# Performance work log

Measured on AMD Instinct MI355X. Metric: run time of the kernel, lower is better.

Reference implementation:

```python
import jax, jax.numpy as jnp
import numpy as np

LATENT, TARGET, EMB_SCALE = 2048, 64, 0.1
STEPS_IGNORE, STEPS_PREDICT = 2, 3


def conv(x, w, b, stride=(1, 1), padding=((0, 0), (0, 0))):
    y = jax.lax.conv_general_dilated(x, w, stride, padding,
                                     dimension_numbers=('NCHW', 'OIHW', 'NCHW'))
    return y + b[None, :, None, None]


def setup_inputs() -> dict:
    key = jax.random.key(0)
    ks = jax.random.split(key, 24)
    B = 64
    inp = {}
    inp['images'] = jax.random.normal(ks[0], (B, 3, 256, 256), jnp.float32)
    inp['rnd'] = jax.random.randint(ks[1], (B * 49,), 0, 16, jnp.int32)
    s = lambda *sh: 1.0 / np.sqrt(np.prod(sh[1:]))
    # stand-in encoder: conv3->256 k8 s8, relu, conv256->2048 1x1, relu, global mean pool
    inp['enc_w1'] = jax.random.normal(ks[2], (256, 3, 8, 8), jnp.float32) * s(256, 3, 8, 8)
    inp['enc_b1'] = jnp.zeros((256,), jnp.float32)
    inp['enc_w2'] = jax.random.normal(ks[3], (LATENT, 256, 1, 1), jnp.float32) * s(LATENT, 256)
    inp['enc_b2'] = jnp.zeros((LATENT,), jnp.float32)
    # PixelCNN: 5 residual blocks, each 4 convs
    inp['pc_w1'] = jax.random.normal(ks[4], (5, 256, LATENT, 1, 1), jnp.float32) * s(0, LATENT)
    inp['pc_b1'] = jnp.zeros((5, 256), jnp.float32)
    inp['pc_w2'] = jax.random.normal(ks[5], (5, 256, 256, 1, 3), jnp.float32) * s(0, 256 * 3)
    inp['pc_b2'] = jnp.zeros((5, 256), jnp.float32)
    inp['pc_w3'] = jax.random.normal(ks[6], (5, 256, 256, 2, 1), jnp.float32) * s(0, 256 * 2)
    inp['pc_b3'] = jnp.zeros((5, 256), jnp.float32)
    inp['pc_w4'] = jax.random.normal(ks[7], (5, LATENT, 256, 1, 1), jnp.float32) * s(0, 256)
    inp['pc_b4'] = jnp.zeros((5, LATENT), jnp.float32)
    inp['z2t_w'] = jax.random.normal(ks[8], (TARGET, LATENT, 1, 1), jnp.float32) * s(0, LATENT)
    inp['z2t_b'] = jnp.zeros((TARGET,), jnp.float32)
    inp['c2p_w'] = jax.random.normal(ks[9], (STEPS_PREDICT, TARGET, LATENT, 1, 1), jnp.float32) * s(0, LATENT)
    inp['c2p_b'] = jnp.zeros((STEPS_PREDICT, TARGET), jnp.float32)
    return inp


def _forward(images, enc_w1, enc_b1, enc_w2, enc_b2,
             pc_w1, pc_b1, pc_w2, pc_b2, pc_w3, pc_b3, pc_w4, pc_b4,
             z2t_w, z2t_b, c2p_w, c2p_b, rnd):
    B = images.shape[0]
    # ---- patch extraction: (B,3,256,256) -> (B*49,3,64,64), r-major then c ----
    patches = jnp.stack([images[:, :, r * 32:r * 32 + 64, c * 32:c * 32 + 64]
                         for r in range(7) for c in range(7)], axis=1)
    patches = patches.reshape(-1, 3, 64, 64)
    N = patches.shape[0]
    # ---- vectorized random border masking (replaces per-patch python loop) ----
    r = (rnd // 4).astype(jnp.int32)           # (N,)
    c = (rnd % 4).astype(jnp.int32)
    idx = jnp.arange(64, dtype=jnp.int32)
    row_ok = (idx[None, :] >= r[:, None]) & (idx[None, :] < r[:, None] + 60)  # (N,64)
    col_ok = (idx[None, :] >= c[:, None]) & (idx[None, :] < c[:, None] + 60)
    mask = row_ok[:, None, :, None] & col_ok[:, None, None, :]                # (N,1,64,64)
    patches = jnp.where(mask, patches, jnp.float32(-1.0))
    # ---- stand-in encoder (resnet_v1 replaced by small conv stack) ----
    h = jax.nn.relu(conv(patches, enc_w1, enc_b1, stride=(8, 8)))  # (N,256,8,8)
    h = jax.nn.relu(conv(h, enc_w2, enc_b2))                        # (N,2048,8,8)
    latents = h.mean(axis=(2, 3))                                   # (N,2048)
    latents = latents.reshape(B, 7, 7, LATENT).transpose(0, 3, 1, 2)  # (B,2048,7,7)
    # ---- PixelCNN context ----
    x = latents
    for k in range(5):
        y = jax.nn.relu(conv(x, pc_w1[k], pc_b1[k]))
        y = jax.nn.relu(conv(y, pc_w2[k], pc_b2[k], padding=((0, 0), (1, 1))))
        y = jax.nn.relu(conv(y, pc_w3[k], pc_b3[k], padding=((1, 0), (0, 0))))
        y = conv(y, pc_w4[k], pc_b4[k])
        x = jax.nn.relu(y + x)
    context = x
    # ---- contrastive loss ----
    targets = conv(latents, z2t_w, z2t_b).transpose(0, 2, 3, 1).reshape(-1, TARGET)  # (B*49,64)
    col_dim, row_dim = 7, 7
    loss = jnp.float32(0.0)
    for i in range(STEPS_IGNORE, STEPS_IGNORE + STEPS_PREDICT):
        col_dim_i = col_dim - i - 1
        total = B * col_dim_i * row_dim
        preds = conv(context, c2p_w[i - STEPS_IGNORE], c2p_b[i - STEPS_IGNORE])
        preds = preds[:, :, :-(i + 1), :] * EMB_SCALE
        preds = preds.transpose(0, 2, 3, 1).reshape(-1, TARGET)  # (total,64)
        logits = preds @ targets.T                                # (total, B*49)
        ar = jnp.arange(total)
        b_idx = ar // (col_dim_i * row_dim)
        col = ar % (col_dim_i * row_dim)
        labels = b_idx * (col_dim * row_dim) + (i + 1) * row_dim + col
        lsm = jax.nn.log_softmax(logits, axis=-1)
        loss = loss + (-lsm[ar, labels]).mean()
    return loss, latents.mean(axis=(2, 3))


def reference(images, rnd, enc_w1, enc_b1, enc_w2, enc_b2,
              pc_w1, pc_b1, pc_w2, pc_b2, pc_w3, pc_b3, pc_w4, pc_b4,
              z2t_w, z2t_b, c2p_w, c2p_b):
    return _forward(images, enc_w1, enc_b1, enc_w2, enc_b2,
                    pc_w1, pc_b1, pc_w2, pc_b2, pc_w3, pc_b3, pc_w4, pc_b4,
                    z2t_w, z2t_b, c2p_w, c2p_b, rnd)
```

## Files before the change

### kernel.cpp

```cpp
#include <hip/hip_runtime.h>
#include <hip/hip_bf16.h>
#include <cstdint>
#include <cstddef>

typedef __attribute__((ext_vector_type(8))) short short8;
typedef __attribute__((ext_vector_type(4))) short short4v;
typedef __attribute__((ext_vector_type(4))) float f32x4;

__device__ __forceinline__ float bf2f(unsigned short u) {
  union { unsigned int i; float f; } v; v.i = ((unsigned int)u) << 16; return v.f;
}
__device__ __forceinline__ unsigned short f2bf(float f) {
  union { float f; unsigned int i; } v; v.f = f;
  unsigned int x = v.i;
  return (unsigned short)((x + 0x7fffu + ((x >> 16) & 1u)) >> 16);
}
__device__ __forceinline__ f32x4 mfma16(short8 a, short8 b, f32x4 c) {
  return __builtin_amdgcn_mfma_f32_16x16x32_bf16(a, b, c, 0, 0, 0);
}
__device__ __forceinline__ void gload16(const void* src, void* dst) {
  __builtin_amdgcn_global_load_lds(
      (const __attribute__((address_space(1))) unsigned int*)src,
      (__attribute__((address_space(3))) unsigned int*)dst, 16, 0, 0);
}

__device__ __forceinline__ void cvt4(const float* __restrict__ src,
                                     unsigned short* __restrict__ dst, int i) {
  float4 v = reinterpret_cast<const float4*>(src)[i];
  short4v o;
  o[0] = (short)f2bf(v.x); o[1] = (short)f2bf(v.y);
  o[2] = (short)f2bf(v.z); o[3] = (short)f2bf(v.w);
  reinterpret_cast<short4v*>(dst)[i] = o;
}

__global__ __launch_bounds__(256) void k_prep(
    const float* __restrict__ enc_w1, const float* __restrict__ enc_w2,
    const float* __restrict__ pc_w1, const float* __restrict__ pc_w4,
    const float* __restrict__ z2t_w, const float* __restrict__ c2p_w,
    const float* __restrict__ pc_w2, const float* __restrict__ pc_w3,
    unsigned short* __restrict__ w1b, unsigned short* __restrict__ w2b,
    unsigned short* __restrict__ pcw1b, unsigned short* __restrict__ pcw4b,
    unsigned short* __restrict__ z2tb, unsigned short* __restrict__ c2pb,
    unsigned short* __restrict__ w2t, unsigned short* __restrict__ w3t)
{
  const int b = blockIdx.x, tid = threadIdx.x;
  if (b < 48)        cvt4(enc_w1, w1b,   b * 256 + tid);
  else if (b < 560)  cvt4(enc_w2, w2b,   (b - 48) * 256 + tid);
  else if (b < 3120) cvt4(pc_w1,  pcw1b, (b - 560) * 256 + tid);
  else if (b < 5680) cvt4(pc_w4,  pcw4b, (b - 3120) * 256 + tid);
  else if (b < 5808) cvt4(z2t_w,  z2tb,  (b - 5680) * 256 + tid);
  else if (b < 6192) cvt4(c2p_w,  c2pb,  (b - 5808) * 256 + tid);
  else if (b < 10032) {
    const int e = (b - 6192) * 256 + tid;
    const int k5 = e / 196608, r = e % 196608;
    const int co = r / 768, kk = r % 768, d = kk >> 8, ci = kk & 255;
    w2t[e] = f2bf(pc_w2[((size_t)(k5 * 256 + co) * 256 + ci) * 3 + d]);
  } else {
    const int e = (b - 10032) * 256 + tid;
    const int k5 = e / 131072, r = e % 131072;
    const int co = r >> 9, kk = r & 511, s = kk >> 8, ci = kk & 255;
    w3t[e] = f2bf(pc_w3[((size_t)(k5 * 256 + co) * 256 + ci) * 2 + s]);
  }
}

__global__ __launch_bounds__(256) void k_enc2(
    const unsigned short* __restrict__ H1, const unsigned short* __restrict__ w2b,
    const float* __restrict__ b2, unsigned short* __restrict__ xout, int gbase)
{
  __shared__ char lds[32768];
  char* At = lds;
  char* Bt = lds + 16384;
  const int tid = threadIdx.x;
  const int nwg = gridDim.x;
  int bid = blockIdx.x;
  int l = bid;
  if ((nwg & 7) == 0) { const int cpx = nwg >> 3; l = (bid & 7) * cpx + (bid >> 3); }
  const int m0 = (l & 15) * 128;
  const int by = l >> 4;
  const int w = tid >> 6, lane = tid & 63, lr = lane & 15, lg = lane >> 4;
  const int wm = w & 1, wn = w >> 1;
  const int srow = lane >> 3, sslot = lane & 7;
  f32x4 acc[4][4];
  for (int i = 0; i < 4; i++) for (int j = 0; j < 4; j++) acc[i][j] = (f32x4)0.f;
  for (int kb = 0; kb < 4; kb++) {
    __syncthreads();
#pragma unroll
    for (int c = 0; c < 4; c++) {
      const int rbase = w * 32 + c * 8;
      const int row = rbase + srow;
      gload16(w2b + (size_t)(m0 + row) * 256 + kb * 64 + ((sslot ^ (row & 7)) * 8),
              At + rbase * 128);
    }
#pragma unroll
    for (int c = 0; c < 4; c++) {
      const int rbase = w * 32 + c * 8;
      const int row = rbase + srow;
      gload16(H1 + (size_t)(by * 128 + row) * 256 + kb * 64 + ((sslot ^ (row & 7)) * 8),
              Bt + rbase * 128);
    }
    __syncthreads();
#pragma unroll
    for (int kk = 0; kk < 2; kk++) {
      const int gg = kk * 4 + lg;
      short8 bb[4];
#pragma unroll
      for (int nt = 0; nt < 4; nt++) {
        const int row = wn * 64 + nt * 16 + lr;
        bb[nt] = *reinterpret_cast<const short8*>(Bt + row * 128 + ((gg ^ (row & 7)) * 16));
      }
#pragma unroll
      for (int cot = 0; cot < 4; cot++) {
        const int row = wm * 64 + cot * 16 + lr;
        const short8 a = *reinterpret_cast<const short8*>(At + row * 128 + ((gg ^ (row & 7)) * 16));
#pragma unroll
        for (int nt = 0; nt < 4; nt++)
          acc[cot][nt] = mfma16(a, bb[nt], acc[cot][nt]);
      }
    }
  }
  const int n = gbase + by * 2 + wn;
#pragma unroll
  for (int cot = 0; cot < 4; cot++) {
    const int cob = m0 + wm * 64 + cot * 16 + lg * 4;
    float4 bi = *reinterpret_cast<const float4*>(b2 + cob);
    const float bv[4] = { bi.x, bi.y, bi.z, bi.w };
    float s[4] = { 0.f, 0.f, 0.f, 0.f };
#pragma unroll
    for (int nt = 0; nt < 4; nt++)
#pragma unroll
      for (int r = 0; r < 4; r++)
        s[r] += fmaxf(acc[cot][nt][r] + bv[r], 0.f);
#pragma unroll
    for (int r = 0; r < 4; r++)
#pragma unroll
      for (int mk = 1; mk < 16; mk <<= 1)
        s[r] += __shfl_xor(s[r], mk, 64);
    if (lr == 0) {
      short4v o;
#pragma unroll
      for (int r = 0; r < 4; r++) o[r] = (short)f2bf(s[r] * (1.f / 64.f));
      *reinterpret_cast<short4v*>(xout + (size_t)n * 2048 + cob) = o;
    }
  }
}

__global__ __launch_bounds__(256) void k_out2(const unsigned short* __restrict__ x,
                                              float* __restrict__ out) {
  const int ch = blockIdx.x * 256 + threadIdx.x;
  const int b = blockIdx.y;
  float s = 0.f;
  for (int p = 0; p < 49; p++) s += bf2f(x[(size_t)(b * 49 + p) * 2048 + ch]);
  out[1 + b * 2048 + ch] = s * (1.f / 49.f);
}

template<int M_BLK, int BK, int MODE, bool BIAS, bool RELU, bool RESID, bool SCALE, bool OBF16>
__global__ __launch_bounds__(256) void k_gemm(
    const unsigned short* __restrict__ in, const unsigned short* __restrict__ W,
    const float* __restrict__ bias, float* __restrict__ outf,
    unsigned short* __restrict__ outb, const unsigned short* __restrict__ res,
    int M, int K, int bstride, int aux, float scale,
    int wzs, int bzs, int ozs,
    const float* __restrict__ img, const int* __restrict__ rndp)
{
  constexpr int MF = M_BLK / 64;
  constexpr int GPR = BK / 8;
  constexpr int ROWS = 64 / GPR;
  constexpr int RS = BK * 2;
  constexpr int CHA = (M_BLK / 4) / ROWS;
  constexpr int CHB = 16 / ROWS;
  constexpr int AG = M_BLK * 8;
  constexpr bool DBUF = (MODE == 0);
  constexpr int BUF = (M_BLK + 64) * RS;
  __shared__ char ldsb[(DBUF ? 2 : 1) * BUF];
  const int tid = threadIdx.x;
  const int z = blockIdx.z;
  W += (size_t)z * wzs;
  if (BIAS) bias += (size_t)z * bzs;
  const int m0 = blockIdx.x * M_BLK;
  const int n0 = blockIdx.y * 64;
  const int w = tid >> 6, lane = tid & 63, lr = lane & 15, lg = lane >> 4;
  const int srow = lane / GPR, sslot = lane % GPR;
  int pb = 0, pR = 0, pC = 0, roff = 0, coff = 0;
  if constexpr (MODE == 4) {
    const int pn = aux + blockIdx.y;
    pb = pn / 49; const int prc = pn % 49; pR = prc / 7; pC = prc % 7;
    const int rv = rndp[pn];
    roff = rv >> 2; coff = rv & 3;
  }
  f32x4 acc[MF][4];
  for (int mf = 0; mf < MF; mf++) for (int nt = 0; nt < 4; nt++) acc[mf][nt] = (f32x4)0.f;
  const int KB = K / BK;

  auto stageA = [&](char* At, int kb) {
#pragma unroll
    for (int c = 0; c < CHA; c++) {
      const int rbase = w * (M_BLK / 4) + c * ROWS;
      const int row = rbase + srow;
      gload16(W + (size_t)(m0 + row) * K + kb * BK + ((sslot ^ (row & 7)) * 8),
              At + rbase * RS);
    }
  };
  auto compute = [&](const char* At, const char* Bt) {
#pragma unroll
    for (int kk = 0; kk < BK / 32; kk++) {
      short8 a[MF], bb[4];
      const int gg = kk * 4 + lg;
#pragma unroll
      for (int mf = 0; mf < MF; mf++) {
        const int row = w * (M_BLK / 4) + mf * 16 + lr;
        a[mf] = *reinterpret_cast<const short8*>(At + row * RS + ((gg ^ (row & 7)) * 16));
      }
#pragma unroll
      for (int nt = 0; nt < 4; nt++) {
        const int row = nt * 16 + lr;
        bb[nt] = *reinterpret_cast<const short8*>(Bt + row * RS + ((gg ^ (row & 7)) * 16));
      }
#pragma unroll
      for (int mf = 0; mf < MF; mf++)
#pragma unroll
        for (int nt = 0; nt < 4; nt++)
          acc[mf][nt] = mfma16(a[mf], bb[nt], acc[mf][nt]);
    }
  };

  if constexpr (DBUF) {
    auto stageB = [&](char* Bt, int kb) {
#pragma unroll
      for (int c = 0; c < CHB; c++) {
        const int rbase = w * 16 + c * ROWS;
        const int row = rbase + srow;
        const int n = n0 + row;
        gload16(in + (size_t)n * bstride + kb * BK + ((sslot ^ (row & 7)) * 8),
                Bt + rbase * RS);
      }
    };
    stageA(ldsb, 0);
    stageB(ldsb + M_BLK * RS, 0);
    __syncthreads();
    int cur = 0;
    for (int kb = 0; kb < KB; kb++) {
      if (kb + 1 < KB) {
        char* nb = ldsb + (cur ^ 1) * BUF;
        stageA(nb, kb + 1);
        stageB(nb + M_BLK * RS, kb + 1);
      }
      char* cb = ldsb + cur * BUF;
      compute(cb, cb + M_BLK * RS);
      __syncthreads();
      cur ^= 1;
    }
  } else {
    for (int kb = 0; kb < KB; kb++) {
      __syncthreads();
      stageA(ldsb, kb);
      char* Bt = ldsb + M_BLK * RS;
      for (int g = AG + tid; g < AG + 512; g += 256) {
        const int h = g - AG, row = h >> 3, slot = h & 7;
        const int n = n0 + row;
        const int k = kb * 64 + slot * 8;
        short8 v = (short8)(short)0;
        if constexpr (MODE == 1) {
          const int d = k >> 8, ci = k & 255;
          const int wp = n % 7 + d - 1;
          if ((unsigned)wp <= 6u)
            v = *reinterpret_cast<const short8*>(in + (size_t)(n + d - 1) * 256 + ci);
        } else if constexpr (MODE == 2) {
          const int s2 = k >> 8, ci = k & 255;
          const int hh = (n % 49) / 7;
          if (hh + s2 >= 1)
            v = *reinterpret_cast<const short8*>(in + (size_t)(n + (s2 - 1) * 7) * 256 + ci);
        } else {
          const int p = row;
          const int gr = kb * 8 + slot;
          const int ci = gr >> 3, ky = gr & 7;
          const int oy = p >> 3, ox = p & 7;
          const int y = oy * 8 + ky;
          const float* src = img + (((size_t)(pb * 3 + ci) * 256 + (size_t)(pR * 32 + y)) * 256
                                    + pC * 32 + ox * 8);
          float4 v0 = *reinterpret_cast<const float4*>(src);
          float4 v1 = *reinterpret_cast<const float4*>(src + 4);
          const bool rok = (y >= roff) && (y < roff + 60);
          float vals[8] = { v0.x, v0.y, v0.z, v0.w, v1.x, v1.y, v1.z, v1.w };
          const int x0 = ox * 8;
#pragma unroll
          for (int q = 0; q < 8; q++) {
            const int xx = x0 + q;
            const bool ok = rok && (xx >= coff) && (xx < coff + 60);
            v[q] = (short)f2bf(ok ? vals[q] : -1.0f);
          }
        }
        *reinterpret_cast<short8*>(Bt + row * RS + ((slot ^ (row & 7)) * 16)) = v;
      }
      __syncthreads();
      compute(ldsb, ldsb + M_BLK * RS);
    }
  }

#pragma unroll
  for (int mf = 0; mf < MF; mf++) {
    const int mb = m0 + w * (M_BLK / 4) + mf * 16 + lg * 4;
    float bv[4] = {0.f, 0.f, 0.f, 0.f};
    if constexpr (BIAS) {
      float4 t4 = *reinterpret_cast<const float4*>(bias + mb);
      bv[0] = t4.x; bv[1] = t4.y; bv[2] = t4.z; bv[3] = t4.w;
    }
#pragma unroll
    for (int nt = 0; nt < 4; nt++) {
      const size_t nn = (size_t)(n0 + nt * 16 + lr);
      const size_t off = nn * (size_t)M + mb + (size_t)z * ozs;
      float v[4];
#pragma unroll
      for (int r = 0; r < 4; r++) {
        v[r] = acc[mf][nt][r] + bv[r];
        if (SCALE) v[r] *= scale;
      }
      if (RESID) {
        short4v rv = *reinterpret_cast<const short4v*>(res + off);
#pragma unroll
        for (int r = 0; r < 4; r++) v[r] += bf2f((unsigned short)rv[r]);
      }
#pragma unroll
      for (int r = 0; r < 4; r++) if (RELU) v[r] = fmaxf(v[r], 0.f);
      if (OBF16) {
        short4v o;
#pragma unroll
        for (int r = 0; r < 4; r++) o[r] = (short)f2bf(v[r]);
        *reinterpret_cast<short4v*>(outb + off) = o;
      } else {
        float4 o; o.x = v[0]; o.y = v[1]; o.z = v[2]; o.w = v[3];
        *reinterpret_cast<float4*>(outf + off) = o;
      }
    }
  }
}

__global__ __launch_bounds__(256) void k_lse2(
    const unsigned short* __restrict__ predsb, const unsigned short* __restrict__ targ,
    float* __restrict__ pm, float* __restrict__ ps, float* __restrict__ zlab)
{
  __shared__ char At[8192];
  __shared__ char Bt[8192];
  __shared__ float redM[4][64], redS[4][64];
  const int tid = threadIdx.x;
  const int R0 = blockIdx.x * 64;
  const int tz = blockIdx.y;
  const int t0 = tz * 13;
  const int t1 = (t0 + 13 < 49) ? (t0 + 13) : 49;
  int ip, base, cd7;
  if (R0 < 1792)      { ip = 0; base = 0;    cd7 = 28; }
  else if (R0 < 3136) { ip = 1; base = 1792; cd7 = 21; }
  else                { ip = 2; base = 3136; cd7 = 14; }
  const int lab7 = 7 * (ip + 3);
  const unsigned short* preds = predsb + (size_t)ip * 200704;
  const int w = tid >> 6, lane = tid & 63, lr = lane & 15, lg = lane >> 4;
  const int srow = lane >> 3, sslot = lane & 7;

#pragma unroll
  for (int c = 0; c < 2; c++) {
    const int rbase = w * 16 + c * 8;
    const int row = rbase + srow;
    const int rr = R0 - base + row;
    const int np = (rr / cd7) * 49 + (rr % cd7);
    gload16(preds + (size_t)np * 64 + ((sslot ^ (row & 7)) * 8), Bt + rbase * 128);
  }

  int labv[4];
#pragma unroll
  for (int nt = 0; nt < 4; nt++) {
    const int nc = R0 - base + nt * 16 + lr;
    labv[nt] = (nc / cd7) * 49 + (nc % cd7) + lab7;
  }
  float mrun[4] = {-1e30f, -1e30f, -1e30f, -1e30f};
  float srun[4] = {0.f, 0.f, 0.f, 0.f};

  for (int t = t0; t < t1; t++) {
#pragma unroll
    for (int c = 0; c < 2; c++) {
      const int rbase = w * 16 + c * 8;
      const int row = rbase + srow;
      gload16(targ + (size_t)(t * 64 + row) * 64 + ((sslot ^ (row & 7)) * 8),
              At + rbase * 128);
    }
    __syncthreads();
    f32x4 av[4];
#pragma unroll
    for (int nt = 0; nt < 4; nt++) av[nt] = (f32x4)0.f;
#pragma unroll
    for (int kk = 0; kk < 2; kk++) {
      const int gg = kk * 4 + lg;
      const int arow = w * 16 + lr;
      const short8 a = *reinterpret_cast<const short8*>(At + arow * 128 + ((gg ^ (arow & 7)) * 16));
#pragma unroll
      for (int nt = 0; nt < 4; nt++) {
        const int brow = nt * 16 + lr;
        const short8 b = *reinterpret_cast<const short8*>(Bt + brow * 128 + ((gg ^ (brow & 7)) * 16));
        av[nt] = mfma16(a, b, av[nt]);
      }
    }
    const int mg = t * 64 + w * 16 + lg * 4;
#pragma unroll
    for (int nt = 0; nt < 4; nt++) {
      float v0 = av[nt][0], v1 = av[nt][1], v2 = av[nt][2], v3 = av[nt][3];
      if (mg + 0 == labv[nt]) zlab[R0 + nt * 16 + lr] = v0;
      if (mg + 1 == labv[nt]) zlab[R0 + nt * 16 + lr] = v1;
      if (mg + 2 == labv[nt]) zlab[R0 + nt * 16 + lr] = v2;
      if (mg + 3 == labv[nt]) zlab[R0 + nt * 16 + lr] = v3;
      const float vm = fmaxf(fmaxf(v0, v1), fmaxf(v2, v3));
      const float nm = fmaxf(mrun[nt], vm);
      srun[nt] = srun[nt] * __expf(mrun[nt] - nm)
               + __expf(v0 - nm) + __expf(v1 - nm) + __expf(v2 - nm) + __expf(v3 - nm);
      mrun[nt] = nm;
    }
    __syncthreads();
  }
#pragma unroll
  for (int nt = 0; nt < 4; nt++) {
#pragma unroll
    for (int mk = 16; mk < 64; mk <<= 1) {
      const float om = __shfl_xor(mrun[nt], mk, 64);
      const float os = __shfl_xor(srun[nt], mk, 64);
      const float nm = fmaxf(mrun[nt], om);
      srun[nt] = srun[nt] * __expf(mrun[nt] - nm) + os * __expf(om - nm);
      mrun[nt] = nm;
    }
    if (lg == 0) { redM[w][nt * 16 + lr] = mrun[nt]; redS[w][nt * 16 + lr] = srun[nt]; }
  }
  __syncthreads();
  if (tid < 64) {
    float m = redM[0][tid], s = redS[0][tid];
#pragma unroll
    for (int wv = 1; wv < 4; wv++) {
      const float om = redM[wv][tid], os = redS[wv][tid];
      const float nm = fmaxf(m, om);
      s = s * __expf(m - nm) + os * __expf(om - nm);
      m = nm;
    }
    pm[(R0 + tid) * 4 + tz] = m;
    ps[(R0 + tid) * 4 + tz] = s;
  }
}

__global__ __launch_bounds__(256) void k_loss_final(
    const float* __restrict__ pm, const float* __restrict__ ps,
    const float* __restrict__ zlab, float* __restrict__ out)
{
  __shared__ float red[256];
  const int tid = threadIdx.x;
  float acc = 0.f;
  for (int i = tid; i < 4032; i += 256) {
    float m = pm[i * 4], s = ps[i * 4];
#pragma unroll
    for (int j = 1; j < 4; j++) {
      const float om = pm[i * 4 + j], os = ps[i * 4 + j];
      const float nm = fmaxf(m, om);
      s = s * __expf(m - nm) + os * __expf(om - nm);
      m = nm;
    }
    const float loss = (m + __logf(s)) - zlab[i];
    const float wgt = (i < 1792) ? (1.f / 1792.f) : ((i < 3136) ? (1.f / 1344.f) : (1.f / 896.f));
    acc += loss * wgt;
  }
  red[tid] = acc;
  for (int off = 128; off > 0; off >>= 1) {
    __syncthreads();
    if (tid < off) red[tid] += red[tid + off];
  }
  if (tid == 0) out[0] = red[0];
}

extern "C" void kernel_launch(void* const* d_in, const int* in_sizes, int n_in,
                              void* d_out, int out_size, void* d_ws, size_t ws_size,
                              hipStream_t stream)
{
  (void)in_sizes; (void)n_in; (void)out_size;
  const float* images = (const float*)d_in[0];
  const int*   rnd    = (const int*)d_in[1];
  const float* enc_w1 = (const float*)d_in[2];
  const float* enc_b1 = (const float*)d_in[3];
  const float* enc_w2 = (const float*)d_in[4];
  const float* enc_b2 = (const float*)d_in[5];
  const float* pc_w1  = (const float*)d_in[6];
  const float* pc_b1  = (const float*)d_in[7];
  const float* pc_w2  = (const float*)d_in[8];
  const float* pc_b2  = (const float*)d_in[9];
  const float* pc_w3  = (const float*)d_in[10];
  const float* pc_b3  = (const float*)d_in[11];
  const float* pc_w4  = (const float*)d_in[12];
  const float* pc_b4  = (const float*)d_in[13];
  const float* z2t_w  = (const float*)d_in[14];
  const float* z2t_b  = (const float*)d_in[15];
  const float* c2p_w  = (const float*)d_in[16];
  const float* c2p_b  = (const float*)d_in[17];
  float* out = (float*)d_out;
  char* ws = (char*)d_ws;

  unsigned short* w1b    = (unsigned short*)(ws + 0);
  unsigned short* w2b    = (unsigned short*)(ws + 98304);
  unsigned short* z2tb   = (unsigned short*)(ws + 1146880);
  unsigned short* c2pb   = (unsigned short*)(ws + 1409024);
  unsigned short* w2t    = (unsigned short*)(ws + 2195456);
  unsigned short* w3t    = (unsigned short*)(ws + 4161536);
  unsigned short* targ   = (unsigned short*)(ws + 5472256);
  unsigned short* predsb = (unsigned short*)(ws + 5873664);
  unsigned short* y1b    = (unsigned short*)(ws + 7094016);
  unsigned short* y2b    = (unsigned short*)(ws + 8699648);
  unsigned short* pcw1b  = (unsigned short*)(ws + 10305280);
  unsigned short* pcw4b  = (unsigned short*)(ws + 15548160);
  unsigned short* xbuf   = (unsigned short*)(ws + 20791040);
  float*          pm     = (float*)(ws + 7094016);
  float*          psum   = (float*)(ws + 7158528);
  float*          zlab   = (float*)(ws + 7223040);

  k_prep<<<12592, 256, 0, stream>>>(enc_w1, enc_w2, pc_w1, pc_w4, z2t_w, c2p_w,
                                    pc_w2, pc_w3,
                                    w1b, w2b, pcw1b, pcw4b, z2tb, c2pb, w2t, w3t);

  const size_t h1_off = 33636352;
  const size_t per_patch = 64 * 256 * 2;
  unsigned short* H1;
  int CH;
  if (ws_size > h1_off + 2 * per_patch) {
    size_t avail = (ws_size - h1_off) / per_patch;
    CH = (int)(avail > 3136 ? 3136 : avail) & ~1;
    H1 = (unsigned short*)(ws + h1_off);
  } else {
    H1 = y1b;
    CH = 98;
  }
  for (int base = 0; base < 3136; base += CH) {
    const int c = (3136 - base) < CH ? (3136 - base) : CH;
    k_gemm<256, 64, 4, true, true, false, false, true><<<dim3(1, c), 256, 0, stream>>>(
        nullptr, w1b, enc_b1, nullptr, H1, nullptr, 256, 192, 0, base, 1.f,
        0, 0, 0, images, rnd);
    k_enc2<<<16 * (c / 2), 256, 0, stream>>>(H1, w2b, enc_b2, xbuf, base);
  }

  k_out2<<<dim3(8, 64), 256, 0, stream>>>(xbuf, out);
  k_gemm<64, 128, 0, true, false, false, false, true><<<dim3(1, 49), 256, 0, stream>>>(
      xbuf, z2tb, z2t_b, nullptr, targ, nullptr, 64, 2048, 2048, 0, 1.f, 0, 0, 0,
      nullptr, nullptr);

  for (int k = 0; k < 5; k++) {
    k_gemm<64, 128, 0, true, true, false, false, true><<<dim3(4, 49), 256, 0, stream>>>(
        xbuf, pcw1b + (size_t)k * 524288, pc_b1 + k * 256, nullptr, y1b, nullptr,
        256, 2048, 2048, 0, 1.f, 0, 0, 0, nullptr, nullptr);
    k_gemm<64, 64, 1, true, true, false, false, true><<<dim3(4, 49), 256, 0, stream>>>(
        y1b, w2t + (size_t)k * 196608, pc_b2 + k * 256, nullptr, y2b, nullptr,
        256, 768, 256, 0, 1.f, 0, 0, 0, nullptr, nullptr);
    k_gemm<64, 64, 2, true, true, false, false, true><<<dim3(4, 49), 256, 0, stream>>>(
        y2b, w3t + (size_t)k * 131072, pc_b3 + k * 256, nullptr, y1b, nullptr,
        256, 512, 256, 0, 1.f, 0, 0, 0, nullptr, nullptr);
    k_gemm<128, 64, 0, true, true, true, false, true><<<dim3(16, 49), 256, 0, stream>>>(
        y1b, pcw4b + (size_t)k * 524288, pc_b4 + k * 2048, nullptr, xbuf, xbuf,
        2048, 256, 256, 0, 1.f, 0, 0, 0, nullptr, nullptr);
  }

  k_gemm<64, 128, 0, true, false, false, true, true><<<dim3(1, 49, 3), 256, 0, stream>>>(
      xbuf, c2pb, c2p_b, nullptr, predsb, nullptr, 64, 2048, 2048, 0, 0.1f,
      131072, 64, 200704, nullptr, nullptr);

  k_lse2<<<dim3(63, 4), 256, 0, stream>>>(predsb, targ, pm, psum, zlab);
  k_loss_final<<<1, 256, 0, stream>>>(pm, psum, zlab, out);
}
```

Baseline: 639.5 us.

## Fuse PixelCNN conv2/conv3 per image, stream enc2 weights from global, widen LSE split

Adds a k_conv23 kernel that computes the 1x3 and 2x1 convolutions for one image in a single block, keeping the intermediate activation in LDS so the y2 global round trip and one launch per residual block go away. In k_enc2 the weight tile is no longer staged through LDS; MFMA A operands are read directly from global memory, which halves LDS use. k_lse2 now splits the target dimension into 7 chunks instead of 4 for more parallelism, and the fallback chunk size for the encoder changes. The fused conv kernel runs only 64 blocks, which may underuse the GPU, and the direct global weight reads rely on cache hits.

Measured after the change: 893.1 us. 39.7% more time.

```diff
diff --git a/kernel.cpp b/kernel.cpp
--- a/kernel.cpp
+++ b/kernel.cpp
@@ -67,9 +67,7 @@
     const unsigned short* __restrict__ H1, const unsigned short* __restrict__ w2b,
     const float* __restrict__ b2, unsigned short* __restrict__ xout, int gbase)
 {
-  __shared__ char lds[32768];
-  char* At = lds;
-  char* Bt = lds + 16384;
+  __shared__ char Bt[16384];
   const int tid = threadIdx.x;
   const int nwg = gridDim.x;
   int bid = blockIdx.x;
@@ -88,13 +86,6 @@
     for (int c = 0; c < 4; c++) {
       const int rbase = w * 32 + c * 8;
       const int row = rbase + srow;
-      gload16(w2b + (size_t)(m0 + row) * 256 + kb * 64 + ((sslot ^ (row & 7)) * 8),
-              At + rbase * 128);
-    }
-#pragma unroll
-    for (int c = 0; c < 4; c++) {
-      const int rbase = w * 32 + c * 8;
-      const int row = rbase + srow;
       gload16(H1 + (size_t)(by * 128 + row) * 256 + kb * 64 + ((sslot ^ (row & 7)) * 8),
               Bt + rbase * 128);
     }
@@ -110,8 +101,9 @@
       }
 #pragma unroll
       for (int cot = 0; cot < 4; cot++) {
-        const int row = wm * 64 + cot * 16 + lr;
-        const short8 a = *reinterpret_cast<const short8*>(At + row * 128 + ((gg ^ (row & 7)) * 16));
+        const int co = m0 + wm * 64 + cot * 16 + lr;
+        const short8 a = *reinterpret_cast<const short8*>(
+            w2b + (size_t)co * 256 + kb * 64 + kk * 32 + lg * 8);
 #pragma unroll
         for (int nt = 0; nt < 4; nt++)
           acc[cot][nt] = mfma16(a, bb[nt], acc[cot][nt]);
@@ -151,6 +143,124 @@
   float s = 0.f;
   for (int p = 0; p < 49; p++) s += bf2f(x[(size_t)(b * 49 + p) * 2048 + ch]);
   out[1 + b * 2048 + ch] = s * (1.f / 49.f);
+}
+
+__global__ __launch_bounds__(256) void k_conv23(
+    const unsigned short* __restrict__ y1, const unsigned short* __restrict__ w2t,
+    const float* __restrict__ b2, const unsigned short* __restrict__ w3t,
+    const float* __restrict__ b3, unsigned short* __restrict__ y3)
+{
+  __shared__ char Bst[8192];
+  __shared__ char y2l[32768];
+  const int tid = threadIdx.x;
+  const int b = blockIdx.x;
+  const int nb = b * 49;
+  const int w = tid >> 6, lane = tid & 63, lr = lane & 15, lg = lane >> 4;
+  f32x4 acc[4][4];
+  for (int i = 0; i < 4; i++) for (int j = 0; j < 4; j++) acc[i][j] = (f32x4)0.f;
+
+  for (int kb = 0; kb < 12; kb++) {
+    __syncthreads();
+    for (int g = tid; g < 512; g += 256) {
+      const int row = g >> 3, slot = g & 7;
+      const int k = kb * 64 + slot * 8;
+      const int d = k >> 8, ci = k & 255;
+      short8 v = (short8)(short)0;
+      if (row < 49) {
+        const int wc = row % 7 + d - 1;
+        if ((unsigned)wc <= 6u)
+          v = *reinterpret_cast<const short8*>(y1 + (size_t)(nb + row + d - 1) * 256 + ci);
+      }
+      *reinterpret_cast<short8*>(Bst + row * 128 + ((slot ^ (row & 7)) * 16)) = v;
+    }
+    __syncthreads();
+#pragma unroll
+    for (int kk = 0; kk < 2; kk++) {
+      const int gg = kk * 4 + lg;
+      short8 bb[4];
+#pragma unroll
+      for (int nt = 0; nt < 4; nt++) {
+        const int row = nt * 16 + lr;
+        bb[nt] = *reinterpret_cast<const short8*>(Bst + row * 128 + ((gg ^ (row & 7)) * 16));
+      }
+#pragma unroll
+      for (int cot = 0; cot < 4; cot++) {
+        const int co = w * 64 + cot * 16 + lr;
+        const short8 a = *reinterpret_cast<const short8*>(
+            w2t + (size_t)co * 768 + kb * 64 + kk * 32 + lg * 8);
+#pragma unroll
+        for (int nt = 0; nt < 4; nt++)
+          acc[cot][nt] = mfma16(a, bb[nt], acc[cot][nt]);
+      }
+    }
+  }
+#pragma unroll
+  for (int cot = 0; cot < 4; cot++) {
+    const int cob = w * 64 + cot * 16 + lg * 4;
+    float4 bi = *reinterpret_cast<const float4*>(b2 + cob);
+    const float bv[4] = { bi.x, bi.y, bi.z, bi.w };
+    const int g2 = cob >> 3;
+#pragma unroll
+    for (int nt = 0; nt < 4; nt++) {
+      const int row = nt * 16 + lr;
+      short4v o;
+#pragma unroll
+      for (int r = 0; r < 4; r++)
+        o[r] = (short)f2bf(fmaxf(acc[cot][nt][r] + bv[r], 0.f));
+      const int sw = (g2 & ~7) | ((g2 & 7) ^ (row & 7));
+      *reinterpret_cast<short4v*>(y2l + row * 512 + sw * 16 + (cob & 7) * 2) = o;
+    }
+  }
+  __syncthreads();
+
+  f32x4 ac2[4][4];
+  for (int i = 0; i < 4; i++) for (int j = 0; j < 4; j++) ac2[i][j] = (f32x4)0.f;
+  for (int kb = 0; kb < 8; kb++) {
+    const int soff = (kb >= 4) ? 0 : -7;
+#pragma unroll
+    for (int kk = 0; kk < 2; kk++) {
+      const int gg = kk * 4 + lg;
+      const int gci = (kb * 8 + gg) & 31;
+      short8 bb[4];
+#pragma unroll
+      for (int nt = 0; nt < 4; nt++) {
+        const int nout = nt * 16 + lr;
+        const int ry = nout + soff;
+        short8 v = (short8)(short)0;
+        if (ry >= 0) {
+          const int sw = (gci & ~7) | ((gci & 7) ^ (ry & 7));
+          v = *reinterpret_cast<const short8*>(y2l + ry * 512 + sw * 16);
+        }
+        bb[nt] = v;
+      }
+#pragma unroll
+      for (int cot = 0; cot < 4; cot++) {
+        const int co = w * 64 + cot * 16 + lr;
+        const short8 a = *reinterpret_cast<const short8*>(
+            w3t + (size_t)co * 512 + kb * 64 + kk * 32 + lg * 8);
+#pragma unroll
+        for (int nt = 0; nt < 4; nt++)
+          ac2[cot][nt] = mfma16(a, bb[nt], ac2[cot][nt]);
+      }
+    }
+  }
+#pragma unroll
+  for (int cot = 0; cot < 4; cot++) {
+    const int cob = w * 64 + cot * 16 + lg * 4;
+    float4 bi = *reinterpret_cast<const float4*>(b3 + cob);
+    const float bv[4] = { bi.x, bi.y, bi.z, bi.w };
+#pragma unroll
+    for (int nt = 0; nt < 4; nt++) {
+      const int nout = nt * 16 + lr;
+      if (nout < 49) {
+        short4v o;
+#pragma unroll
+        for (int r = 0; r < 4; r++)
+          o[r] = (short)f2bf(fmaxf(ac2[cot][nt][r] + bv[r], 0.f));
+        *reinterpret_cast<short4v*>(y3 + (size_t)(nb + nout) * 256 + cob) = o;
+      }
+    }
+  }
 }
 
 template<int M_BLK, int BK, int MODE, bool BIAS, bool RELU, bool RESID, bool SCALE, bool OBF16>
@@ -256,20 +366,8 @@
       char* Bt = ldsb + M_BLK * RS;
       for (int g = AG + tid; g < AG + 512; g += 256) {
         const int h = g - AG, row = h >> 3, slot = h & 7;
-        const int n = n0 + row;
-        const int k = kb * 64 + slot * 8;
         short8 v = (short8)(short)0;
-        if constexpr (MODE == 1) {
-          const int d = k >> 8, ci = k & 255;
-          const int wp = n % 7 + d - 1;
-          if ((unsigned)wp <= 6u)
-            v = *reinterpret_cast<const short8*>(in + (size_t)(n + d - 1) * 256 + ci);
-        } else if constexpr (MODE == 2) {
-          const int s2 = k >> 8, ci = k & 255;
-          const int hh = (n % 49) / 7;
-          if (hh + s2 >= 1)
-            v = *reinterpret_cast<const short8*>(in + (size_t)(n + (s2 - 1) * 7) * 256 + ci);
-        } else {
+        {
           const int p = row;
           const int gr = kb * 8 + slot;
           const int ci = gr >> 3, ky = gr & 7;
@@ -344,8 +442,8 @@
   const int tid = threadIdx.x;
   const int R0 = blockIdx.x * 64;
   const int tz = blockIdx.y;
-  const int t0 = tz * 13;
-  const int t1 = (t0 + 13 < 49) ? (t0 + 13) : 49;
+  const int t0 = tz * 7;
+  const int t1 = t0 + 7;
   int ip, base, cd7;
   if (R0 < 1792)      { ip = 0; base = 0;    cd7 = 28; }
   else if (R0 < 3136) { ip = 1; base = 1792; cd7 = 21; }
@@ -435,8 +533,8 @@
       s = s * __expf(m - nm) + os * __expf(om - nm);
       m = nm;
     }
-    pm[(R0 + tid) * 4 + tz] = m;
-    ps[(R0 + tid) * 4 + tz] = s;
+    pm[(R0 + tid) * 7 + tz] = m;
+    ps[(R0 + tid) * 7 + tz] = s;
   }
 }
 
@@ -448,10 +546,10 @@
   const int tid = threadIdx.x;
   float acc = 0.f;
   for (int i = tid; i < 4032; i += 256) {
-    float m = pm[i * 4], s = ps[i * 4];
-#pragma unroll
-    for (int j = 1; j < 4; j++) {
-      const float om = pm[i * 4 + j], os = ps[i * 4 + j];
+    float m = pm[i * 7], s = ps[i * 7];
+#pragma unroll
+    for (int j = 1; j < 7; j++) {
+      const float om = pm[i * 7 + j], os = ps[i * 7 + j];
       const float nm = fmaxf(m, om);
       s = s * __expf(m - nm) + os * __expf(om - nm);
       m = nm;
@@ -503,13 +601,12 @@
   unsigned short* targ   = (unsigned short*)(ws + 5472256);
   unsigned short* predsb = (unsigned short*)(ws + 5873664);
   unsigned short* y1b    = (unsigned short*)(ws + 7094016);
-  unsigned short* y2b    = (unsigned short*)(ws + 8699648);
   unsigned short* pcw1b  = (unsigned short*)(ws + 10305280);
   unsigned short* pcw4b  = (unsigned short*)(ws + 15548160);
   unsigned short* xbuf   = (unsigned short*)(ws + 20791040);
   float*          pm     = (float*)(ws + 7094016);
-  float*          psum   = (float*)(ws + 7158528);
-  float*          zlab   = (float*)(ws + 7223040);
+  float*          psum   = (float*)(ws + 7206912);
+  float*          zlab   = (float*)(ws + 7319808);
 
   k_prep<<<12592, 256, 0, stream>>>(enc_w1, enc_w2, pc_w1, pc_w4, z2t_w, c2p_w,
                                     pc_w2, pc_w3,
@@ -525,7 +622,7 @@
     H1 = (unsigned short*)(ws + h1_off);
   } else {
     H1 = y1b;
-    CH = 98;
+    CH = 48;
   }
   for (int base = 0; base < 3136; base += CH) {
     const int c = (3136 - base) < CH ? (3136 - base) : CH;
@@ -544,12 +641,9 @@
     k_gemm<64, 128, 0, true, true, false, false, true><<<dim3(4, 49), 256, 0, stream>>>(
         xbuf, pcw1b + (size_t)k * 524288, pc_b1 + k * 256, nullptr, y1b, nullptr,
         256, 2048, 2048, 0, 1.f, 0, 0, 0, nullptr, nullptr);
-    k_gemm<64, 64, 1, true, true, false, false, true><<<dim3(4, 49), 256, 0, stream>>>(
-        y1b, w2t + (size_t)k * 196608, pc_b2 + k * 256, nullptr, y2b, nullptr,
-        256, 768, 256, 0, 1.f, 0, 0, 0, nullptr, nullptr);
-    k_gemm<64, 64, 2, true, true, false, false, true><<<dim3(4, 49), 256, 0, stream>>>(
-        y2b, w3t + (size_t)k * 131072, pc_b3 + k * 256, nullptr, y1b, nullptr,
-        256, 512, 256, 0, 1.f, 0, 0, 0, nullptr, nullptr);
+    k_conv23<<<64, 256, 0, stream>>>(
+        y1b, w2t + (size_t)k * 196608, pc_b2 + k * 256,
+        w3t + (size_t)k * 131072, pc_b3 + k * 256, y1b);
     k_gemm<128, 64, 0, true, true, true, false, true><<<dim3(16, 49), 256, 0, stream>>>(
         y1b, pcw4b + (size_t)k * 524288, pc_b4 + k * 2048, nullptr, xbuf, xbuf,
         2048, 256, 256, 0, 1.f, 0, 0, 0, nullptr, nullptr);
@@ -559,6 +653,6 @@
       xbuf, c2pb, c2p_b, nullptr, predsb, nullptr, 64, 2048, 2048, 0, 0.1f,
       131072, 64, 200704, nullptr, nullptr);
 
-  k_lse2<<<dim3(63, 4), 256, 0, stream>>>(predsb, targ, pm, psum, zlab);
+  k_lse2<<<dim3(63, 7), 256, 0, stream>>>(predsb, targ, pm, psum, zlab);
   k_loss_final<<<1, 256, 0, stream>>>(pm, psum, zlab, out);
 }
```
